# Performance work log

Hardware: AMD Instinct MI355X
Metric: run time of the kernel (lower is better)

## Reference

```python
import jax, jax.numpy as jnp
import numpy as np

N = 100000
E = 1600000
NIN = 128
NOUT = 128


def setup_inputs() -> dict:
    key = jax.random.key(0)
    k1, k2, k3, k4 = jax.random.split(key, 4)
    x = jax.random.normal(k1, (N, NIN), dtype=jnp.float32)
    edge_index = jax.random.randint(k2, (2, E), 0, N, dtype=jnp.int64)
    edge_attr = jnp.ones((E,), dtype=jnp.float32)  # unused by GCNConv
    # PyG Linear weight is [out, in]; glorot-ish init
    W = jax.random.normal(k3, (NOUT, NIN), dtype=jnp.float32) / np.sqrt(NIN)
    b = jnp.zeros((NOUT,), dtype=jnp.float32)
    return {"x": x, "edge_index": edge_index, "edge_attr": edge_attr, "W": W, "b": b}


def reference(x, edge_index, edge_attr, W, b):
    # PyG GCNConv: add self-loops, symmetric degree normalization,
    # linear transform, scatter-add aggregation at destination, + bias.
    n = x.shape[0]
    loops = jnp.arange(n, dtype=edge_index.dtype)
    src = jnp.concatenate([edge_index[0], loops])  # [E+N]
    dst = jnp.concatenate([edge_index[1], loops])  # [E+N]
    # degree over destination (col) including self-loops, edge weight = 1
    deg = jax.ops.segment_sum(jnp.ones_like(dst, dtype=x.dtype), dst, num_segments=n)
    dinv = jnp.where(deg > 0, jax.lax.rsqrt(deg), 0.0)
    norm = dinv[src] * dinv[dst]  # [E+N]
    h = x @ W.T  # [N, NOUT]
    msg = h[src] * norm[:, None]  # [E+N, NOUT]
    out = jax.ops.segment_sum(msg, dst, num_segments=n)  # [N, NOUT]
    return out + b
```

## Files before the change

### kernel.cpp

```cpp
#include <hip/hip_runtime.h>

#define TPB 256
#define NBLK 256
#define BSH 8

typedef __attribute__((ext_vector_type(4))) float f32x4;
typedef __attribute__((ext_vector_type(8))) short short8;

__device__ __forceinline__ unsigned short f2bf(float f) {
    unsigned u = __float_as_uint(f);
    u = (u + 0x7fffu + ((u >> 16) & 1u)) >> 16;
    return (unsigned short)u;
}
__device__ __forceinline__ float bflo(unsigned u) { return __uint_as_float(u << 16); }
__device__ __forceinline__ float bfhi(unsigned u) { return __uint_as_float(u & 0xffff0000u); }


__global__ __launch_bounds__(256) void k_bhist(const int* __restrict__ dst,
                                               int* __restrict__ blockhist, int E) {
    __shared__ int sh[512];
    int t = threadIdx.x;
    sh[t] = 0; sh[t + 256] = 0;
    __syncthreads();
    int chunk = (E + NBLK - 1) / NBLK;
    int lo = blockIdx.x * chunk;
    int hi = min(E, lo + chunk);
    for (int e = lo + t; e < hi; e += 256)
        atomicAdd(&sh[dst[e] >> BSH], 1);
    __syncthreads();
    int* row = blockhist + blockIdx.x * 512;
    row[t] = sh[t];
    row[t + 256] = sh[t + 256];
}


__global__ __launch_bounds__(512) void k_bscan(const int* __restrict__ blockhist,
                                               int* __restrict__ bbase, int* __restrict__ bcur,
                                               int* __restrict__ offsets, int E, int N) {
    __shared__ int tmp[2][512];
    int t = threadIdx.x;
    int total = 0;
    #pragma unroll 8
    for (int b = 0; b < NBLK; ++b) total += blockhist[b * 512 + t];
    tmp[0][t] = total;
    __syncthreads();
    int sb = 0;
    for (int d = 1; d < 512; d <<= 1) {
        int val = tmp[sb][t] + ((t >= d) ? tmp[sb][t - d] : 0);
        tmp[sb ^ 1][t] = val;
        sb ^= 1;
        __syncthreads();
    }
    int excl = tmp[sb][t] - total;
    bbase[t] = excl;
    bcur[t] = excl;
    if (t == 0) { bbase[512] = E; offsets[N] = E; }
}


__global__ __launch_bounds__(256) void k_bscatter(const int* __restrict__ src,
                                                  const int* __restrict__ dst,
                                                  int* __restrict__ bcur,
                                                  int2* __restrict__ pairs, int E, int NB) {
    __shared__ int sh[512];
    __shared__ int sbase[512];
    int t = threadIdx.x;
    sh[t] = 0; sh[t + 256] = 0;
    __syncthreads();
    int chunk = (E + NBLK - 1) / NBLK;
    int lo = blockIdx.x * chunk;
    int hi = min(E, lo + chunk);
    for (int e = lo + t; e < hi; e += 256)
        atomicAdd(&sh[dst[e] >> BSH], 1);
    __syncthreads();
    for (int i = t; i < NB; i += 256) {
        int c = sh[i];
        sbase[i] = c ? atomicAdd(&bcur[i], c) : 0;
    }
    __syncthreads();
    for (int i = t; i < NB; i += 256) sh[i] = sbase[i];
    __syncthreads();
    for (int e = lo + t; e < hi; e += 256) {
        int d = dst[e];
        int pos = atomicAdd(&sh[d >> BSH], 1);
        pairs[pos] = make_int2(d, src[e]);
    }
}


__global__ __launch_bounds__(256) void k_bcsr(const int2* __restrict__ pairs,
                                              const int* __restrict__ bbase,
                                              int* __restrict__ offsets,
                                              int* __restrict__ sorted_src,
                                              float* __restrict__ dinv, int N) {
    __shared__ int hist[256];
    __shared__ int tmp[2][256];
    __shared__ int scur[256];
    int b = blockIdx.x;
    int s0 = bbase[b], s1 = bbase[b + 1];
    int t = threadIdx.x;
    hist[t] = 0;
    __syncthreads();
    for (int e = s0 + t; e < s1; e += 256)
        atomicAdd(&hist[pairs[e].x & 255], 1);
    __syncthreads();
    int v = hist[t];
    tmp[0][t] = v;
    __syncthreads();
    int sb = 0;
    for (int d = 1; d < 256; d <<= 1) {
        int val = tmp[sb][t] + ((t >= d) ? tmp[sb][t - d] : 0);
        tmp[sb ^ 1][t] = val;
        sb ^= 1;
        __syncthreads();
    }
    int gbase = s0 + (tmp[sb][t] - v);
    scur[t] = gbase;
    int d = (b << BSH) + t;
    if (d < N) { offsets[d] = gbase; dinv[d] = rsqrtf((float)v + 1.0f); }
    __syncthreads();
    for (int e = s0 + t; e < s1; e += 256) {
        int2 pr = pairs[e];
        int pos = atomicAdd(&scur[pr.x & 255], 1);
        sorted_src[pos] = pr.y;
    }
}


__global__ __launch_bounds__(256) void k_gemm(const float* __restrict__ x,
                                              const float* __restrict__ W,
                                              const float* __restrict__ dinv,
                                              unsigned short* __restrict__ g, int n) {
    __shared__ unsigned short wb[128][136];
    const int tid = threadIdx.x;

    for (int chunk = tid; chunk < 2048; chunk += 256) {
        int nrow = chunk >> 4, k8 = (chunk & 15) << 3;
        const float* wp = W + nrow * 128 + k8;
        float4 w0 = *(const float4*)wp;
        float4 w1 = *(const float4*)(wp + 4);
        union { unsigned short u[8]; uint4 q; } pk;
        pk.u[0] = f2bf(w0.x); pk.u[1] = f2bf(w0.y); pk.u[2] = f2bf(w0.z); pk.u[3] = f2bf(w0.w);
        pk.u[4] = f2bf(w1.x); pk.u[5] = f2bf(w1.y); pk.u[6] = f2bf(w1.z); pk.u[7] = f2bf(w1.w);
        *(uint4*)&wb[nrow][k8] = pk.q;
    }
    __syncthreads();

    const int lane = tid & 63;
    const int wid  = tid >> 6;
    const int l15  = lane & 15;
    const int quad = lane >> 4;
    const int row  = blockIdx.x * 64 + wid * 16 + l15;
    const int rowc = (row < n) ? row : (n - 1);

    f32x4 acc[8];
    #pragma unroll
    for (int t = 0; t < 8; ++t) acc[t] = (f32x4){0.f, 0.f, 0.f, 0.f};

    #pragma unroll
    for (int ks = 0; ks < 4; ++ks) {
        const int kb = ks * 32 + quad * 8;
        float4 a0 = *(const float4*)(x + (long)rowc * 128 + kb);
        float4 a1 = *(const float4*)(x + (long)rowc * 128 + kb + 4);
        union { unsigned short u[8]; short8 v; } af;
        af.u[0] = f2bf(a0.x); af.u[1] = f2bf(a0.y); af.u[2] = f2bf(a0.z); af.u[3] = f2bf(a0.w);
        af.u[4] = f2bf(a1.x); af.u[5] = f2bf(a1.y); af.u[6] = f2bf(a1.z); af.u[7] = f2bf(a1.w);
        #pragma unroll
        for (int t = 0; t < 8; ++t) {
            short8 bf = *(const short8*)&wb[t * 16 + l15][kb];
            acc[t] = __builtin_amdgcn_mfma_f32_16x16x32_bf16(af.v, bf, acc[t], 0, 0, 0);
        }
    }

    int   orow[4];
    float dv[4];
    #pragma unroll
    for (int r = 0; r < 4; ++r) {
        orow[r] = blockIdx.x * 64 + wid * 16 + quad * 4 + r;
        dv[r]   = (orow[r] < n) ? dinv[orow[r]] : 0.f;
    }
    #pragma unroll
    for (int t = 0; t < 8; ++t) {
        int col = t * 16 + l15;
        #pragma unroll
        for (int r = 0; r < 4; ++r) {
            if (orow[r] < n)
                g[(long)orow[r] * 128 + col] = f2bf(acc[t][r] * dv[r]);
        }
    }
}


__global__ __launch_bounds__(256) void k_aggregate(const int* __restrict__ sorted_src,
                                                   const int* __restrict__ offsets,
                                                   const unsigned short* __restrict__ g,
                                                   const float* __restrict__ dinv,
                                                   const float* __restrict__ b,
                                                   float* __restrict__ out, int n) {
    int d = blockIdx.x * (TPB / 32) + (threadIdx.x >> 5);
    if (d >= n) return;
    int c = (threadIdx.x & 31) << 2;

    int s0 = offsets[d];
    int s1 = offsets[d + 1];

    float4 acc = make_float4(0.f, 0.f, 0.f, 0.f);
    auto addrow = [&](int r) {
        uint2 p = *(const uint2*)(g + (long)r * 128 + c);
        acc.x += bflo(p.x); acc.y += bfhi(p.x);
        acc.z += bflo(p.y); acc.w += bfhi(p.y);
    };

    addrow(d);
    int e = s0;
    for (; e + 16 <= s1; e += 16) {
        int a[16];
        #pragma unroll
        for (int j = 0; j < 16; ++j) a[j] = sorted_src[e + j];
        #pragma unroll
        for (int j = 0; j < 16; ++j) addrow(a[j]);
    }
    for (; e + 4 <= s1; e += 4) {
        int a[4];
        #pragma unroll
        for (int j = 0; j < 4; ++j) a[j] = sorted_src[e + j];
        #pragma unroll
        for (int j = 0; j < 4; ++j) addrow(a[j]);
    }
    for (; e < s1; ++e) addrow(sorted_src[e]);

    float s = dinv[d];
    float4 bb = *(const float4*)(b + c);
    float4 r = make_float4(acc.x * s + bb.x, acc.y * s + bb.y,
                           acc.z * s + bb.z, acc.w * s + bb.w);
    *(float4*)(out + (long)d * 128 + c) = r;
}


extern "C" void kernel_launch(void* const* d_in, const int* in_sizes, int n_in,
                              void* d_out, int out_size, void* d_ws, size_t ws_size,
                              hipStream_t stream) {
    const float* x  = (const float*)d_in[0];
    const int*   ei = (const int*)d_in[1];
    const float* W  = (const float*)d_in[3];
    const float* b  = (const float*)d_in[4];
    float* out = (float*)d_out;

    const int N = in_sizes[0] / 128;
    const int E = in_sizes[1] / 2;
    const int* src = ei;
    const int* dst = ei + E;
    const int NB = (N + 255) >> BSH;

    char* p = (char*)d_ws;
    auto carve = [&](size_t bytes) { char* q = p; p += (bytes + 255) & ~(size_t)255; return q; };
    int*            blockhist  = (int*)           carve((size_t)NBLK * 512 * 4);
    int*            bbase      = (int*)           carve(513 * 4);
    int*            bcur       = (int*)           carve(512 * 4);
    int*            offsets    = (int*)           carve((size_t)(N + 1) * 4);
    float*          dinv       = (float*)         carve((size_t)N * 4);
    int2*           pairs      = (int2*)          carve((size_t)E * 8);
    int*            sorted_src = (int*)           carve((size_t)E * 4);
    unsigned short* g          = (unsigned short*)carve((size_t)N * 128 * 2);

    k_bhist   <<<NBLK, TPB, 0, stream>>>(dst, blockhist, E);
    k_bscan   <<<1, 512, 0, stream>>>(blockhist, bbase, bcur, offsets, E, N);
    k_bscatter<<<NBLK, TPB, 0, stream>>>(src, dst, bcur, pairs, E, NB);
    k_bcsr    <<<NB, TPB, 0, stream>>>(pairs, bbase, offsets, sorted_src, dinv, N);

    k_gemm<<<(N + 63) / 64, TPB, 0, stream>>>(x, W, dinv, g, N);

    k_aggregate<<<(N + (TPB / 32) - 1) / (TPB / 32), TPB, 0, stream>>>(
        sorted_src, offsets, g, dinv, b, out, N);
}
```

Measured before the change: 254.9 us.

## Use per-block scanned histograms in scatter and pack edge pairs into one word

The bucket scan now writes a per-block exclusive prefix back into blockhist. The scatter kernel can then take its start offsets directly, which removes its second histogram pass and its global atomics on bcur. Each (dst,src) pair is packed into a 32-bit word (src<<8 | dst&255), halving the intermediate buffer traffic. The aggregation inner unroll also drops from 16 to 8. The packing assumes src fits in 24 bits, and the single-block scan now does a serial read-modify-write over blockhist.

```diff
diff --git a/kernel.cpp b/kernel.cpp
--- a/kernel.cpp
+++ b/kernel.cpp
@@ -34,15 +34,17 @@
 }
 
 
-__global__ __launch_bounds__(512) void k_bscan(const int* __restrict__ blockhist,
-                                               int* __restrict__ bbase, int* __restrict__ bcur,
-                                               int* __restrict__ offsets, int E, int N) {
+__global__ __launch_bounds__(512) void k_bscan(int* __restrict__ blockhist,
+                                               int* __restrict__ bbase, int E) {
     __shared__ int tmp[2][512];
     int t = threadIdx.x;
-    int total = 0;
-    #pragma unroll 8
-    for (int b = 0; b < NBLK; ++b) total += blockhist[b * 512 + t];
-    tmp[0][t] = total;
+    int run = 0;
+    for (int b = 0; b < NBLK; ++b) {
+        int v = blockhist[b * 512 + t];
+        blockhist[b * 512 + t] = run;
+        run += v;
+    }
+    tmp[0][t] = run;
     __syncthreads();
     int sb = 0;
     for (int d = 1; d < 512; d <<= 1) {
@@ -51,48 +53,38 @@
         sb ^= 1;
         __syncthreads();
     }
-    int excl = tmp[sb][t] - total;
-    bbase[t] = excl;
-    bcur[t] = excl;
-    if (t == 0) { bbase[512] = E; offsets[N] = E; }
+    bbase[t] = tmp[sb][t] - run;
+    if (t == 0) bbase[512] = E;
 }
 
 
 __global__ __launch_bounds__(256) void k_bscatter(const int* __restrict__ src,
                                                   const int* __restrict__ dst,
-                                                  int* __restrict__ bcur,
-                                                  int2* __restrict__ pairs, int E, int NB) {
+                                                  const int* __restrict__ blockhist,
+                                                  const int* __restrict__ bbase,
+                                                  unsigned* __restrict__ packed, int E) {
     __shared__ int sh[512];
-    __shared__ int sbase[512];
-    int t = threadIdx.x;
-    sh[t] = 0; sh[t + 256] = 0;
+    int t = threadIdx.x;
+    const int* row = blockhist + blockIdx.x * 512;
+    sh[t]       = bbase[t]       + row[t];
+    sh[t + 256] = bbase[t + 256] + row[t + 256];
     __syncthreads();
     int chunk = (E + NBLK - 1) / NBLK;
     int lo = blockIdx.x * chunk;
     int hi = min(E, lo + chunk);
-    for (int e = lo + t; e < hi; e += 256)
-        atomicAdd(&sh[dst[e] >> BSH], 1);
-    __syncthreads();
-    for (int i = t; i < NB; i += 256) {
-        int c = sh[i];
-        sbase[i] = c ? atomicAdd(&bcur[i], c) : 0;
-    }
-    __syncthreads();
-    for (int i = t; i < NB; i += 256) sh[i] = sbase[i];
-    __syncthreads();
     for (int e = lo + t; e < hi; e += 256) {
         int d = dst[e];
         int pos = atomicAdd(&sh[d >> BSH], 1);
-        pairs[pos] = make_int2(d, src[e]);
-    }
-}
-
-
-__global__ __launch_bounds__(256) void k_bcsr(const int2* __restrict__ pairs,
+        packed[pos] = ((unsigned)src[e] << 8) | (unsigned)(d & 255);
+    }
+}
+
+
+__global__ __launch_bounds__(256) void k_bcsr(const unsigned* __restrict__ packed,
                                               const int* __restrict__ bbase,
                                               int* __restrict__ offsets,
                                               int* __restrict__ sorted_src,
-                                              float* __restrict__ dinv, int N) {
+                                              float* __restrict__ dinv, int N, int E) {
     __shared__ int hist[256];
     __shared__ int tmp[2][256];
     __shared__ int scur[256];
@@ -102,7 +94,7 @@
     hist[t] = 0;
     __syncthreads();
     for (int e = s0 + t; e < s1; e += 256)
-        atomicAdd(&hist[pairs[e].x & 255], 1);
+        atomicAdd(&hist[packed[e] & 255u], 1);
     __syncthreads();
     int v = hist[t];
     tmp[0][t] = v;
@@ -118,11 +110,12 @@
     scur[t] = gbase;
     int d = (b << BSH) + t;
     if (d < N) { offsets[d] = gbase; dinv[d] = rsqrtf((float)v + 1.0f); }
+    if (b == 0 && t == 0) offsets[N] = E;
     __syncthreads();
     for (int e = s0 + t; e < s1; e += 256) {
-        int2 pr = pairs[e];
-        int pos = atomicAdd(&scur[pr.x & 255], 1);
-        sorted_src[pos] = pr.y;
+        unsigned pk = packed[e];
+        int pos = atomicAdd(&scur[pk & 255u], 1);
+        sorted_src[pos] = (int)(pk >> 8);
     }
 }
 
@@ -213,12 +206,12 @@
 
     addrow(d);
     int e = s0;
-    for (; e + 16 <= s1; e += 16) {
-        int a[16];
-        #pragma unroll
-        for (int j = 0; j < 16; ++j) a[j] = sorted_src[e + j];
-        #pragma unroll
-        for (int j = 0; j < 16; ++j) addrow(a[j]);
+    for (; e + 8 <= s1; e += 8) {
+        int a[8];
+        #pragma unroll
+        for (int j = 0; j < 8; ++j) a[j] = sorted_src[e + j];
+        #pragma unroll
+        for (int j = 0; j < 8; ++j) addrow(a[j]);
     }
     for (; e + 4 <= s1; e += 4) {
         int a[4];
@@ -256,17 +249,16 @@
     auto carve = [&](size_t bytes) { char* q = p; p += (bytes + 255) & ~(size_t)255; return q; };
     int*            blockhist  = (int*)           carve((size_t)NBLK * 512 * 4);
     int*            bbase      = (int*)           carve(513 * 4);
-    int*            bcur       = (int*)           carve(512 * 4);
     int*            offsets    = (int*)           carve((size_t)(N + 1) * 4);
     float*          dinv       = (float*)         carve((size_t)N * 4);
-    int2*           pairs      = (int2*)          carve((size_t)E * 8);
+    unsigned*       packed     = (unsigned*)      carve((size_t)E * 4);
     int*            sorted_src = (int*)           carve((size_t)E * 4);
     unsigned short* g          = (unsigned short*)carve((size_t)N * 128 * 2);
 
     k_bhist   <<<NBLK, TPB, 0, stream>>>(dst, blockhist, E);
-    k_bscan   <<<1, 512, 0, stream>>>(blockhist, bbase, bcur, offsets, E, N);
-    k_bscatter<<<NBLK, TPB, 0, stream>>>(src, dst, bcur, pairs, E, NB);
-    k_bcsr    <<<NB, TPB, 0, stream>>>(pairs, bbase, offsets, sorted_src, dinv, N);
+    k_bscan   <<<1, 512, 0, stream>>>(blockhist, bbase, E);
+    k_bscatter<<<NBLK, TPB, 0, stream>>>(src, dst, blockhist, bbase, packed, E);
+    k_bcsr    <<<NB, TPB, 0, stream>>>(packed, bbase, offsets, sorted_src, dinv, N, E);
 
     k_gemm<<<(N + 63) / 64, TPB, 0, stream>>>(x, W, dinv, g, N);
 
```

Measured after the change: 253.6 us. No clear change (-0.5%).
